# Kernel optimization log

Measured on AMD Instinct MI355X. Metric: run time of the kernel, lower is better.

Reference implementation:

```python
import jax, jax.numpy as jnp
import numpy as np

N = 100000   # num_nodes
E = 1600000  # num_edges
R = 8        # num_rels
B = 4        # num_bases
D = 64       # inp_dim = h_dim = out_dim


def setup_inputs() -> dict:
    key = jax.random.key(0)
    ks = jax.random.split(key, 16)
    s = 1.0 / np.sqrt(D)
    inp = {
        'h': jax.random.normal(ks[0], (N, D), jnp.float32),
        'src': jax.random.randint(ks[1], (E,), 0, N),
        'dst': jax.random.randint(ks[2], (E,), 0, N),
        'etype': jax.random.randint(ks[3], (E,), 0, R),
        'norm': jax.random.uniform(ks[4], (E, 1), jnp.float32),
    }
    for i in range(3):  # i2h, hidden, h2o layers (basis decomposition)
        inp[f'bases{i}'] = jax.random.normal(ks[5 + 2 * i], (B, D, D), jnp.float32) * s
        inp[f'wcomp{i}'] = jax.random.normal(ks[6 + 2 * i], (R, B), jnp.float32) * s
    inp['dec_w1'] = jax.random.normal(ks[11], (D, D), jnp.float32) * s
    inp['dec_b1'] = jnp.zeros((D,), jnp.float32)
    inp['dec_w2'] = jax.random.normal(ks[12], (D, 1), jnp.float32) * s
    inp['dec_b2'] = jnp.zeros((1,), jnp.float32)
    return inp


def rgcn_layer(h, src, dst, etype, norm, bases, wcomp, activate):
    # basis decomposition: W_r = sum_b wcomp[r,b] * bases[b]
    W = jnp.einsum('rb,bio->rio', wcomp, bases)           # [R, D, D]
    # transform all nodes under every relation (dense GEMM), then gather per edge
    Ht = jnp.einsum('ni,rio->rno', h, W).reshape(R * N, -1)  # [R*N, D]
    msg = Ht[etype * N + src] * norm                      # [E, D] gather + norm
    out = jax.ops.segment_sum(msg, dst, num_segments=N)   # scatter-add to dst
    return jax.nn.relu(out) if activate else out


def reference(h, src, dst, etype, norm, bases0, wcomp0, bases1, wcomp1,
              bases2, wcomp2, dec_w1, dec_b1, dec_w2, dec_b2):
    # EncoderRGCN: i2h (relu) -> hidden (relu) -> h2o (no activation)
    h1 = rgcn_layer(h, src, dst, etype, norm, bases0, wcomp0, True)
    h2 = rgcn_layer(h1, src, dst, etype, norm, bases1, wcomp1, True)
    henc = rgcn_layer(h2, src, dst, etype, norm, bases2, wcomp2, False)
    # AttributeDecoder: Linear -> ReLU -> Linear(reconstruct_dim=1)
    d1 = jax.nn.relu(henc @ dec_w1 + dec_b1)
    rec = (d1 @ dec_w2 + dec_b2).squeeze()                # [N]
    return rec, henc
```

## Files before the change

kernel.cpp:

```cpp
#include <hip/hip_runtime.h>

typedef _Float16 half8 __attribute__((ext_vector_type(8)));
typedef _Float16 half4 __attribute__((ext_vector_type(4)));
typedef _Float16 half2v __attribute__((ext_vector_type(2)));
typedef float floatx4 __attribute__((ext_vector_type(4)));

constexpr int NN = 100000;
constexpr int EE = 1600000;
constexpr int NBK = 196;
constexpr int CHUNK = 3125;
constexpr int CAPB = 12288;
constexpr int NDCAP = 48;

__global__ __launch_bounds__(512) void k_part(const int* __restrict__ dst,
                                              const int* __restrict__ src,
                                              const int* __restrict__ etype,
                                              const float* __restrict__ norm,
                                              int* __restrict__ gcur,
                                              int2* __restrict__ part) {
  __shared__ int2 ldata[CHUNK];
  __shared__ unsigned char lbkt[CHUNK];
  __shared__ int lhist[NBK], lbase[NBK + 1], lcur[NBK], gbase[NBK];
  __shared__ int sh[256];
  const int tid = threadIdx.x;
  const int e0 = blockIdx.x * CHUNK;

  if (tid < NBK) lhist[tid] = 0;
  __syncthreads();
  for (int i = tid; i < CHUNK; i += 512)
    atomicAdd(&lhist[dst[e0 + i] >> 9], 1);
  __syncthreads();
  {
    const int v = (tid < NBK) ? lhist[tid] : 0;
    if (tid < 256) sh[tid] = v;
    __syncthreads();
    int run = v;
    for (int d = 1; d < 256; d <<= 1) {
      const int t = (tid >= d && tid < 256) ? sh[tid - d] : 0;
      __syncthreads();
      run += t;
      if (tid < 256) sh[tid] = run;
      __syncthreads();
    }
    if (tid < NBK) {
      lbase[tid] = run - v;
      lcur[tid] = 0;
      gbase[tid] = tid * CAPB + atomicAdd(&gcur[tid], v);
    }
    if (tid == 0) lbase[NBK] = CHUNK;
  }
  __syncthreads();
  for (int i = tid; i < CHUNK; i += 512) {
    const int e = e0 + i;
    const int d = dst[e], s = src[e], et = etype[e];
    const _Float16 nh = (_Float16)norm[e];
    const unsigned short n16 = __builtin_bit_cast(unsigned short, nh);
    const int bk = d >> 9;
    const int pos = lbase[bk] + atomicAdd(&lcur[bk], 1);
    ldata[pos] = make_int2((d << 15) | (s >> 2), (s & 3) | (et << 2) | ((int)n16 << 5));
    lbkt[pos] = (unsigned char)bk;
  }
  __syncthreads();
  for (int i = tid; i < CHUNK; i += 512) {
    const int bk = (int)lbkt[i];
    part[gbase[bk] + (i - lbase[bk])] = ldata[i];
  }
}

__global__ __launch_bounds__(1024) void k_part2(const int* __restrict__ gcur,
                                                const int2* __restrict__ part,
                                                int* __restrict__ off,
                                                int2* __restrict__ em) {
  __shared__ int hcnt[512];
  __shared__ int wred[16];
  __shared__ int swsum[8];
  const int tid = threadIdx.x;
  const int bk = blockIdx.x;
  const int nb0 = bk << 9;
  const int2* __restrict__ pp = part + (size_t)bk * CAPB;

  {
    int pv = (tid < bk) ? gcur[tid] : 0;
    for (int d = 32; d > 0; d >>= 1) pv += __shfl_down(pv, d);
    if ((tid & 63) == 0) wred[tid >> 6] = pv;
  }
  if (tid < 512) hcnt[tid] = 0;
  __syncthreads();
  int base = 0;
#pragma unroll
  for (int w = 0; w < 16; ++w) base += wred[w];
  const int cntb = gcur[bk];

  for (int i = tid; i < cntb; i += 1024)
    atomicAdd(&hcnt[(((unsigned)pp[i].x) >> 15) & 511], 1);
  __syncthreads();
  const int v = (tid < 512) ? hcnt[tid] : 0;
  int incl = v;
  for (int d = 1; d < 64; d <<= 1) {
    const int t = __shfl_up(incl, d);
    if ((tid & 63) >= d) incl += t;
  }
  if (tid < 512 && (tid & 63) == 63) swsum[tid >> 6] = incl;
  __syncthreads();
  if (tid < 512) {
    int pre = 0;
    for (int w = 0; w < (tid >> 6); ++w) pre += swsum[w];
    const int excl = pre + incl - v;
    const int n = nb0 + tid;
    if (n < NN) off[n] = base + excl;
    hcnt[tid] = excl;
  }
  if (bk == NBK - 1 && tid == 0) off[NN] = EE;
  __syncthreads();
  for (int i = tid; i < cntb; i += 1024) {
    const int2 r = pp[i];
    const int d = ((unsigned)r.x) >> 15;
    const int s = ((r.x & 0x7FFF) << 2) | (r.y & 3);
    const int et = (r.y >> 2) & 7;
    const unsigned short n16 = (unsigned short)((r.y >> 5) & 0xFFFF);
    const float nf = (float)__builtin_bit_cast(_Float16, n16);
    const int pos = atomicAdd(&hcnt[d & 511], 1);
    em[base + pos] = make_int2(((d & 15) << 23) | (et << 20) | s, __float_as_int(nf));
  }
}


__global__ __launch_bounds__(256) void k_prep(const float* __restrict__ h,
                                              _Float16* __restrict__ hh,
                                              const float* __restrict__ b0,
                                              const float* __restrict__ b1,
                                              const float* __restrict__ b2,
                                              _Float16* __restrict__ bbt,
                                              int* __restrict__ gcur) {
  const int bx = blockIdx.x;
  if (bx == 0 && threadIdx.x < NBK) gcur[threadIdx.x] = 0;
  if (bx < 6250) {
    const int i = bx * 256 + threadIdx.x;
    const float4 v = *(const float4*)&h[(size_t)i * 4];
    half4 o = {(_Float16)v.x, (_Float16)v.y, (_Float16)v.z, (_Float16)v.w};
    *(half4*)&hh[(size_t)i * 4] = o;
  } else {
    const int g = (bx - 6250) >> 6;
    const int idx = ((bx - 6250) & 63) * 256 + threadIdx.x;
    const float* bases = (g == 0) ? b0 : (g == 1) ? b1 : b2;
    const int o = idx >> 8, k = idx & 255;
    const int b = k >> 6, i = k & 63;
    bbt[g * 16384 + idx] = (_Float16)bases[b * 4096 + i * 64 + o];
  }
}

__global__ __launch_bounds__(256, 8) void k_layer(const _Float16* __restrict__ hh,
                                                  const int* __restrict__ off,
                                                  const int2* __restrict__ em,
                                                  const float* __restrict__ wcomp,
                                                  const _Float16* __restrict__ bbt,
                                                  _Float16* __restrict__ out16,
                                                  float* __restrict__ out32) {
  __shared__ _Float16 Ash[16 * 264];
  __shared__ int  ems_s[16 * NDCAP];
  __shared__ int2 ems_c[16 * NDCAP];
  __shared__ float4 wcs[8];
  __shared__ int offs[17];
  __shared__ int ovf;
  const int tid = threadIdx.x;
  const int lane = tid & 63;
  const int wv = tid >> 6;
  const int n0 = blockIdx.x * 16;

  if (tid < 17) offs[tid] = off[n0 + tid];
  if (tid == 0) ovf = 0;
  if (tid < 8) wcs[tid] = ((const float4*)wcomp)[tid];
  {
    const int4 z4 = make_int4(0, 0, 0, 0);
    int4* zs = (int4*)ems_s;
    int4* zc = (int4*)ems_c;
    if (tid < 192) zs[tid] = z4;
    for (int i = tid; i < 384; i += 256) zc[i] = z4;
  }
  __syncthreads();

  const int e0 = offs[0];
  const int len = offs[16] - e0;
  for (int i = tid; i < len; i += 256) {
    const int g = e0 + i;
    const int2 r = em[g];
    const int lo = (r.x >> 23) & 15;
    const int rank = g - offs[lo];
    const int et = (r.x >> 20) & 7;
    const int s = r.x & 0xFFFFF;
    const float nf = __int_as_float(r.y);
    const float4 w = wcs[et];
    const _Float16 c0 = (_Float16)(nf * w.x), c1 = (_Float16)(nf * w.y);
    const _Float16 c2 = (_Float16)(nf * w.z), c3 = (_Float16)(nf * w.w);
    const half2v p01 = {c0, c1}, p23 = {c2, c3};
    if (rank < NDCAP) {
      ems_s[lo * NDCAP + rank] = s;
      ems_c[lo * NDCAP + rank] = make_int2(
          __builtin_bit_cast(int, p01), __builtin_bit_cast(int, p23));
    } else ovf = 1;
  }
  __syncthreads();

#define LOADB(mm, bb, hv)                                                      \
  {                                                                            \
    const int4* sp4_ = (const int4*)&ems_s[(mm) * NDCAP + (bb) * 16 + eg * 8]; \
    const int4 sa_ = sp4_[0], sb_ = sp4_[1];                                   \
    hv[0] = hp[(unsigned)sa_.x * 32u + fl];                                    \
    hv[1] = hp[(unsigned)sa_.y * 32u + fl];                                    \
    hv[2] = hp[(unsigned)sa_.z * 32u + fl];                                    \
    hv[3] = hp[(unsigned)sa_.w * 32u + fl];                                    \
    hv[4] = hp[(unsigned)sb_.x * 32u + fl];                                    \
    hv[5] = hp[(unsigned)sb_.y * 32u + fl];                                    \
    hv[6] = hp[(unsigned)sb_.z * 32u + fl];                                    \
    hv[7] = hp[(unsigned)sb_.w * 32u + fl];                                    \
  }

#define FMAQ(mm, bb, hv, aq)                                                   \
  {                                                                            \
    const int4* cp4_ = (const int4*)&ems_c[(mm) * NDCAP + (bb) * 16 + eg * 8]; \
    _Pragma("unroll")                                                          \
    for (int k_ = 0; k_ < 4; ++k_) {                                           \
      const int4 c_ = cp4_[k_];                                                \
      const half2v pa01_ = __builtin_bit_cast(half2v, c_.x);                   \
      const half2v pa23_ = __builtin_bit_cast(half2v, c_.y);                   \
      const half2v pb01_ = __builtin_bit_cast(half2v, c_.z);                   \
      const half2v pb23_ = __builtin_bit_cast(half2v, c_.w);                   \
      aq[0] = aq[0] + hv[2 * k_] * __builtin_shufflevector(pa01_, pa01_, 0, 0);\
      aq[1] = aq[1] + hv[2 * k_] * __builtin_shufflevector(pa01_, pa01_, 1, 1);\
      aq[2] = aq[2] + hv[2 * k_] * __builtin_shufflevector(pa23_, pa23_, 0, 0);\
      aq[3] = aq[3] + hv[2 * k_] * __builtin_shufflevector(pa23_, pa23_, 1, 1);\
      aq[0] = aq[0] + hv[2 * k_ + 1] * __builtin_shufflevector(pb01_, pb01_, 0, 0);\
      aq[1] = aq[1] + hv[2 * k_ + 1] * __builtin_shufflevector(pb01_, pb01_, 1, 1);\
      aq[2] = aq[2] + hv[2 * k_ + 1] * __builtin_shufflevector(pb23_, pb23_, 0, 0);\
      aq[3] = aq[3] + hv[2 * k_ + 1] * __builtin_shufflevector(pb23_, pb23_, 1, 1);\
    }                                                                          \
  }

  if (!ovf) {
    const int fl = lane & 31;
    const int eg = lane >> 5;
    const half2v* __restrict__ hp = (const half2v*)hh;
    const int mb = wv * 4;
    const int oA = offs[mb], oB = offs[mb + 1], oC = offs[mb + 2],
              oD = offs[mb + 3], oE = offs[mb + 4];
    const int c0n = oB - oA, c1n = oC - oB, c2n = oD - oC, c3n = oE - oD;
    const int nb0_ = (c0n > 0) ? ((c0n + 15) >> 4) : 1;
    const int nb1_ = (c1n > 0) ? ((c1n + 15) >> 4) : 1;
    const int nb2_ = (c2n > 0) ? ((c2n + 15) >> 4) : 1;
    const int nb3_ = (c3n > 0) ? ((c3n + 15) >> 4) : 1;

    half2v acc[4][4];
#pragma unroll
    for (int q = 0; q < 4; ++q)
#pragma unroll
      for (int i = 0; i < 4; ++i) acc[q][i] = half2v{0, 0};

    half2v hvA[8], hvB[8];
    LOADB(mb, 0, hvA);
#pragma unroll
    for (int q = 0; q < 4; ++q) {
      const int m = mb + q;
      const int nbq = (q == 0) ? nb0_ : (q == 1) ? nb1_ : (q == 2) ? nb2_ : nb3_;
      if (q < 3) {
        if (q & 1) LOADB(m + 1, 0, hvA) else LOADB(m + 1, 0, hvB)
      }
      if (q & 1) FMAQ(m, 0, hvB, acc[q]) else FMAQ(m, 0, hvA, acc[q])
      for (int b = 1; b < nbq; ++b) {
        if (q & 1) {
          LOADB(m, b, hvB) FMAQ(m, b, hvB, acc[q])
        } else {
          LOADB(m, b, hvA) FMAQ(m, b, hvA, acc[q])
        }
      }
    }
#pragma unroll
    for (int q = 0; q < 4; ++q) {
      const int m = mb + q;
#pragma unroll
      for (int i = 0; i < 4; ++i)
        acc[q][i] = acc[q][i] + __builtin_bit_cast(half2v,
            __shfl_xor(__builtin_bit_cast(int, acc[q][i]), 32));
      if (eg == 0) {
        _Float16* ar = &Ash[m * 264];
        *(half2v*)&ar[0 * 64 + 2 * fl] = acc[q][0];
        *(half2v*)&ar[1 * 64 + 2 * fl] = acc[q][1];
        *(half2v*)&ar[2 * 64 + 2 * fl] = acc[q][2];
        *(half2v*)&ar[3 * 64 + 2 * fl] = acc[q][3];
      }
    }
  } else {
    const _Float16* hl = hh + lane;
    for (int q = 0; q < 4; ++q) {
      const int m = wv * 4 + q;
      const int p0 = offs[m], p1 = offs[m + 1];
      float a0 = 0.f, a1 = 0.f, a2 = 0.f, a3 = 0.f;
      for (int p = p0; p < p1; p += 8) {
#pragma unroll
        for (int j = 0; j < 8; ++j) {
          const bool live = (p + j < p1);
          const int idx = live ? p + j : p1 - 1;
          const int2 mm = em[idx];
          const float hv = (float)hl[(size_t)(mm.x & 0xFFFFF) << 6];
          const float wn = live ? __int_as_float(mm.y) : 0.f;
          const float4 w = wcs[(mm.x >> 20) & 7];
          const float t = wn * hv;
          a0 = fmaf(t, w.x, a0); a1 = fmaf(t, w.y, a1);
          a2 = fmaf(t, w.z, a2); a3 = fmaf(t, w.w, a3);
        }
      }
      _Float16* ar = &Ash[m * 264];
      ar[lane]       = (_Float16)a0;
      ar[64 + lane]  = (_Float16)a1;
      ar[128 + lane] = (_Float16)a2;
      ar[192 + lane] = (_Float16)a3;
    }
  }
  __syncthreads();

  const int col = lane & 15;
  const int quad = lane >> 4;
  const int obase = wv * 16 + col;
  const _Float16* ap = &Ash[col * 264 + quad * 8];
  const _Float16* bp = &bbt[(size_t)obase * 256 + quad * 8];
  floatx4 acc2 = {0.f, 0.f, 0.f, 0.f};
#pragma unroll
  for (int s = 0; s < 8; ++s) {
    const half8 af = *(const half8*)(ap + s * 32);
    const half8 bf = *(const half8*)(bp + s * 32);
    acc2 = __builtin_amdgcn_mfma_f32_16x16x32_f16(af, bf, acc2, 0, 0, 0);
  }
  if (out16) {
#pragma unroll
    for (int r = 0; r < 4; ++r) {
      const float c = fmaxf(acc2[r], 0.f);
      out16[(size_t)(n0 + quad * 4 + r) * 64 + obase] = (_Float16)c;
    }
  } else {
#pragma unroll
    for (int r = 0; r < 4; ++r) {
      out32[(size_t)(n0 + quad * 4 + r) * 64 + obase] = acc2[r];
    }
  }
#undef LOADB
#undef FMAQ
}

__global__ __launch_bounds__(256) void k_dec(const float* __restrict__ henc,
                                             const float* __restrict__ w1,
                                             const float* __restrict__ b1,
                                             const float* __restrict__ w2,
                                             const float* __restrict__ b2,
                                             float* __restrict__ rec) {
  __shared__ float w1s[64 * 64];
  __shared__ float hs[16 * 68];
  const int tid = threadIdx.x;
  for (int r = tid; r < 1024; r += 256)
    *(float4*)&w1s[r * 4] = *(const float4*)&w1[r * 4];
  const int og = tid & 15;
  const int nl = tid >> 4;
  const float4 wv2 = *(const float4*)&w2[og * 4];
  const float4 bv1 = *(const float4*)&b1[og * 4];
  const float b2v = b2[0];
  for (int t0 = blockIdx.x * 16; t0 < NN; t0 += gridDim.x * 16) {
    __syncthreads();
    {
      const float4 hv = *(const float4*)&henc[(size_t)t0 * 64 + tid * 4];
      *(float4*)&hs[(tid >> 4) * 68 + (tid & 15) * 4] = hv;
    }
    __syncthreads();
    float4 acc = bv1;
    const float* hr = &hs[nl * 68];
#pragma unroll 8
    for (int i = 0; i < 64; ++i) {
      const float hv = hr[i];
      const float4 wv = *(const float4*)&w1s[i * 64 + og * 4];
      acc.x = fmaf(hv, wv.x, acc.x); acc.y = fmaf(hv, wv.y, acc.y);
      acc.z = fmaf(hv, wv.z, acc.z); acc.w = fmaf(hv, wv.w, acc.w);
    }
    acc.x = fmaxf(acc.x, 0.f); acc.y = fmaxf(acc.y, 0.f);
    acc.z = fmaxf(acc.z, 0.f); acc.w = fmaxf(acc.w, 0.f);
    float v = acc.x * wv2.x + acc.y * wv2.y + acc.z * wv2.z + acc.w * wv2.w;
    v += __shfl_xor(v, 1); v += __shfl_xor(v, 2);
    v += __shfl_xor(v, 4); v += __shfl_xor(v, 8);
    if (og == 0) rec[t0 + nl] = v + b2v;
  }
}


extern "C" void kernel_launch(void* const* d_in, const int* in_sizes, int n_in,
                              void* d_out, int out_size, void* d_ws, size_t ws_size,
                              hipStream_t stream) {
  const float* h     = (const float*)d_in[0];
  const int*   src   = (const int*)d_in[1];
  const int*   dst   = (const int*)d_in[2];
  const int*   etype = (const int*)d_in[3];
  const float* norm  = (const float*)d_in[4];
  const float* bases[3] = {(const float*)d_in[5], (const float*)d_in[7], (const float*)d_in[9]};
  const float* wcomp[3] = {(const float*)d_in[6], (const float*)d_in[8], (const float*)d_in[10]};
  const float* dw1 = (const float*)d_in[11];
  const float* db1 = (const float*)d_in[12];
  const float* dw2 = (const float*)d_in[13];
  const float* db2 = (const float*)d_in[14];

  float* rec  = (float*)d_out;
  float* henc = (float*)d_out + NN;

  char* ws = (char*)d_ws;
  int*      off    = (int*)(ws + 0);
  int*      gcur   = (int*)(ws + 400512);
  int2*     em     = (int2*)(ws + 402560);
  _Float16* hh     = (_Float16*)(ws + 13202560);
  _Float16* h1f    = (_Float16*)(ws + 26002560);
  _Float16* h2f    = (_Float16*)(ws + 38802560);
  _Float16* bbt    = (_Float16*)(ws + 51602560);
  int2*     part   = (int2*)h1f;

  k_prep<<<6250 + 192, 256, 0, stream>>>(h, hh, bases[0], bases[1], bases[2], bbt, gcur);

  k_part<<<512, 512, 0, stream>>>(dst, src, etype, norm, gcur, part);
  k_part2<<<NBK, 1024, 0, stream>>>(gcur, part, off, em);

  k_layer<<<NN / 16, 256, 0, stream>>>(hh,  off, em, wcomp[0], bbt,         h1f, nullptr);
  k_layer<<<NN / 16, 256, 0, stream>>>(h1f, off, em, wcomp[1], bbt + 16384, h2f, nullptr);
  k_layer<<<NN / 16, 256, 0, stream>>>(h2f, off, em, wcomp[2], bbt + 32768, nullptr, henc);

  k_dec<<<1024, 256, 0, stream>>>(henc, dw1, db1, dw2, db2, rec);
}
```

Before: 322.5 us.

## Triple-buffer edge gathers across nodes with fully unrolled static schedule

Replaces the per-node loop, which kept two gather buffers in flight, with a fully unrolled schedule that keeps three register buffers in flight. Node batches interleave, so the gather loads for one batch overlap the FMAs of another. The new code handles at most three 16-edge batches per node, which relies on the NDCAP=48 limit and the overflow fallback. Launch bounds drop from 8 to 6 waves per unit to make room for the extra registers, trading occupancy for more memory-level parallelism in each wave.

```diff
diff --git a/kernel.cpp b/kernel.cpp
--- a/kernel.cpp
+++ b/kernel.cpp
@@ -149,7 +149,7 @@
   }
 }
 
-__global__ __launch_bounds__(256, 8) void k_layer(const _Float16* __restrict__ hh,
+__global__ __launch_bounds__(256, 6) void k_layer(const _Float16* __restrict__ hh,
                                                   const int* __restrict__ off,
                                                   const int2* __restrict__ em,
                                                   const float* __restrict__ wcomp,
@@ -201,39 +201,43 @@
   }
   __syncthreads();
 
-#define LOADB(mm, bb, hv)                                                      \
+#define LOADB(mm, bb, P)                                                       \
   {                                                                            \
     const int4* sp4_ = (const int4*)&ems_s[(mm) * NDCAP + (bb) * 16 + eg * 8]; \
     const int4 sa_ = sp4_[0], sb_ = sp4_[1];                                   \
-    hv[0] = hp[(unsigned)sa_.x * 32u + fl];                                    \
-    hv[1] = hp[(unsigned)sa_.y * 32u + fl];                                    \
-    hv[2] = hp[(unsigned)sa_.z * 32u + fl];                                    \
-    hv[3] = hp[(unsigned)sa_.w * 32u + fl];                                    \
-    hv[4] = hp[(unsigned)sb_.x * 32u + fl];                                    \
-    hv[5] = hp[(unsigned)sb_.y * 32u + fl];                                    \
-    hv[6] = hp[(unsigned)sb_.z * 32u + fl];                                    \
-    hv[7] = hp[(unsigned)sb_.w * 32u + fl];                                    \
-  }
-
-#define FMAQ(mm, bb, hv, aq)                                                   \
+    P##0 = hp[(unsigned)sa_.x * 32u + fl];                                     \
+    P##1 = hp[(unsigned)sa_.y * 32u + fl];                                     \
+    P##2 = hp[(unsigned)sa_.z * 32u + fl];                                     \
+    P##3 = hp[(unsigned)sa_.w * 32u + fl];                                     \
+    P##4 = hp[(unsigned)sb_.x * 32u + fl];                                     \
+    P##5 = hp[(unsigned)sb_.y * 32u + fl];                                     \
+    P##6 = hp[(unsigned)sb_.z * 32u + fl];                                     \
+    P##7 = hp[(unsigned)sb_.w * 32u + fl];                                     \
+  }
+
+#define FMA2(hx, hy, cc, qi)                                                   \
+  {                                                                            \
+    const half2v pa01_ = __builtin_bit_cast(half2v, cc.x);                     \
+    const half2v pa23_ = __builtin_bit_cast(half2v, cc.y);                     \
+    const half2v pb01_ = __builtin_bit_cast(half2v, cc.z);                     \
+    const half2v pb23_ = __builtin_bit_cast(half2v, cc.w);                     \
+    acc[qi][0] = acc[qi][0] + hx * __builtin_shufflevector(pa01_, pa01_, 0, 0);\
+    acc[qi][1] = acc[qi][1] + hx * __builtin_shufflevector(pa01_, pa01_, 1, 1);\
+    acc[qi][2] = acc[qi][2] + hx * __builtin_shufflevector(pa23_, pa23_, 0, 0);\
+    acc[qi][3] = acc[qi][3] + hx * __builtin_shufflevector(pa23_, pa23_, 1, 1);\
+    acc[qi][0] = acc[qi][0] + hy * __builtin_shufflevector(pb01_, pb01_, 0, 0);\
+    acc[qi][1] = acc[qi][1] + hy * __builtin_shufflevector(pb01_, pb01_, 1, 1);\
+    acc[qi][2] = acc[qi][2] + hy * __builtin_shufflevector(pb23_, pb23_, 0, 0);\
+    acc[qi][3] = acc[qi][3] + hy * __builtin_shufflevector(pb23_, pb23_, 1, 1);\
+  }
+
+#define FMAQ(mm, bb, P, qi)                                                    \
   {                                                                            \
     const int4* cp4_ = (const int4*)&ems_c[(mm) * NDCAP + (bb) * 16 + eg * 8]; \
-    _Pragma("unroll")                                                          \
-    for (int k_ = 0; k_ < 4; ++k_) {                                           \
-      const int4 c_ = cp4_[k_];                                                \
-      const half2v pa01_ = __builtin_bit_cast(half2v, c_.x);                   \
-      const half2v pa23_ = __builtin_bit_cast(half2v, c_.y);                   \
-      const half2v pb01_ = __builtin_bit_cast(half2v, c_.z);                   \
-      const half2v pb23_ = __builtin_bit_cast(half2v, c_.w);                   \
-      aq[0] = aq[0] + hv[2 * k_] * __builtin_shufflevector(pa01_, pa01_, 0, 0);\
-      aq[1] = aq[1] + hv[2 * k_] * __builtin_shufflevector(pa01_, pa01_, 1, 1);\
-      aq[2] = aq[2] + hv[2 * k_] * __builtin_shufflevector(pa23_, pa23_, 0, 0);\
-      aq[3] = aq[3] + hv[2 * k_] * __builtin_shufflevector(pa23_, pa23_, 1, 1);\
-      aq[0] = aq[0] + hv[2 * k_ + 1] * __builtin_shufflevector(pb01_, pb01_, 0, 0);\
-      aq[1] = aq[1] + hv[2 * k_ + 1] * __builtin_shufflevector(pb01_, pb01_, 1, 1);\
-      aq[2] = aq[2] + hv[2 * k_ + 1] * __builtin_shufflevector(pb23_, pb23_, 0, 0);\
-      aq[3] = aq[3] + hv[2 * k_ + 1] * __builtin_shufflevector(pb23_, pb23_, 1, 1);\
-    }                                                                          \
+    const int4 c0_ = cp4_[0]; FMA2(P##0, P##1, c0_, qi)                        \
+    const int4 c1_ = cp4_[1]; FMA2(P##2, P##3, c1_, qi)                        \
+    const int4 c2_ = cp4_[2]; FMA2(P##4, P##5, c2_, qi)                        \
+    const int4 c3_ = cp4_[3]; FMA2(P##6, P##7, c3_, qi)                        \
   }
 
   if (!ovf) {
@@ -244,10 +248,8 @@
     const int oA = offs[mb], oB = offs[mb + 1], oC = offs[mb + 2],
               oD = offs[mb + 3], oE = offs[mb + 4];
     const int c0n = oB - oA, c1n = oC - oB, c2n = oD - oC, c3n = oE - oD;
-    const int nb0_ = (c0n > 0) ? ((c0n + 15) >> 4) : 1;
-    const int nb1_ = (c1n > 0) ? ((c1n + 15) >> 4) : 1;
-    const int nb2_ = (c2n > 0) ? ((c2n + 15) >> 4) : 1;
-    const int nb3_ = (c3n > 0) ? ((c3n + 15) >> 4) : 1;
+    const bool v1_0 = c0n > 16, v1_1 = c1n > 16, v1_2 = c2n > 16, v1_3 = c3n > 16;
+    const bool v2_0 = c0n > 32, v2_1 = c1n > 32, v2_2 = c2n > 32, v2_3 = c3n > 32;
 
     half2v acc[4][4];
 #pragma unroll
@@ -255,24 +257,35 @@
 #pragma unroll
       for (int i = 0; i < 4; ++i) acc[q][i] = half2v{0, 0};
 
-    half2v hvA[8], hvB[8];
-    LOADB(mb, 0, hvA);
-#pragma unroll
-    for (int q = 0; q < 4; ++q) {
-      const int m = mb + q;
-      const int nbq = (q == 0) ? nb0_ : (q == 1) ? nb1_ : (q == 2) ? nb2_ : nb3_;
-      if (q < 3) {
-        if (q & 1) LOADB(m + 1, 0, hvA) else LOADB(m + 1, 0, hvB)
-      }
-      if (q & 1) FMAQ(m, 0, hvB, acc[q]) else FMAQ(m, 0, hvA, acc[q])
-      for (int b = 1; b < nbq; ++b) {
-        if (q & 1) {
-          LOADB(m, b, hvB) FMAQ(m, b, hvB, acc[q])
-        } else {
-          LOADB(m, b, hvA) FMAQ(m, b, hvA, acc[q])
-        }
-      }
-    }
+    half2v x0, x1, x2, x3, x4, x5, x6, x7;
+    half2v y0, y1, y2, y3, y4, y5, y6, y7;
+    half2v z0, z1, z2, z3, z4, z5, z6, z7;
+
+    LOADB(mb + 0, 0, x)
+    LOADB(mb + 1, 0, y)
+    LOADB(mb + 2, 0, z)
+    FMAQ(mb + 0, 0, x, 0)
+    LOADB(mb + 3, 0, x)
+    FMAQ(mb + 1, 0, y, 1)
+    if (v1_0) LOADB(mb + 0, 1, y)
+    FMAQ(mb + 2, 0, z, 2)
+    if (v1_1) LOADB(mb + 1, 1, z)
+    FMAQ(mb + 3, 0, x, 3)
+    if (v1_2) LOADB(mb + 2, 1, x)
+    if (v1_0) FMAQ(mb + 0, 1, y, 0)
+    if (v1_3) LOADB(mb + 3, 1, y)
+    if (v1_1) FMAQ(mb + 1, 1, z, 1)
+    if (v2_0) LOADB(mb + 0, 2, z)
+    if (v1_2) FMAQ(mb + 2, 1, x, 2)
+    if (v2_1) LOADB(mb + 1, 2, x)
+    if (v1_3) FMAQ(mb + 3, 1, y, 3)
+    if (v2_2) LOADB(mb + 2, 2, y)
+    if (v2_0) FMAQ(mb + 0, 2, z, 0)
+    if (v2_3) LOADB(mb + 3, 2, z)
+    if (v2_1) FMAQ(mb + 1, 2, x, 1)
+    if (v2_2) FMAQ(mb + 2, 2, y, 2)
+    if (v2_3) FMAQ(mb + 3, 2, z, 3)
+
 #pragma unroll
     for (int q = 0; q < 4; ++q) {
       const int m = mb + q;
@@ -342,6 +355,7 @@
     }
   }
 #undef LOADB
+#undef FMA2
 #undef FMAQ
 }
 
```

Result: slower. 841.6 us (+161.0%).

## Replace two-pass bucketed CSR build with atomic histogram, scan, and placement

Applied to the files above, without the earlier changes.

Drops the two-stage bucket partition (per-block local sort into 196 dst buckets, then a per-bucket counting sort) that built the dst-sorted edge list. In its place are a global atomic degree histogram, a two-kernel prefix scan, and an atomic-cursor placement kernel. The new path trades shared-memory staging and coalesced writes for simpler kernels. It adds many global atomics on the degree and cursor arrays and scattered 8-byte writes to em. Edge order within a node is no longer deterministic, so floating-point accumulation order can vary between runs.

```diff
diff --git a/kernel.cpp b/kernel.cpp
--- a/kernel.cpp
+++ b/kernel.cpp
@@ -7,120 +7,68 @@
 
 constexpr int NN = 100000;
 constexpr int EE = 1600000;
-constexpr int NBK = 196;
-constexpr int CHUNK = 3125;
-constexpr int CAPB = 12288;
 constexpr int NDCAP = 48;
 
-__global__ __launch_bounds__(512) void k_part(const int* __restrict__ dst,
-                                              const int* __restrict__ src,
-                                              const int* __restrict__ etype,
-                                              const float* __restrict__ norm,
-                                              int* __restrict__ gcur,
-                                              int2* __restrict__ part) {
-  __shared__ int2 ldata[CHUNK];
-  __shared__ unsigned char lbkt[CHUNK];
-  __shared__ int lhist[NBK], lbase[NBK + 1], lcur[NBK], gbase[NBK];
-  __shared__ int sh[256];
+
+__global__ __launch_bounds__(256) void k_hist(const int* __restrict__ dst,
+                                              int* __restrict__ deg) {
+  for (int e = blockIdx.x * 256 + threadIdx.x; e < EE; e += gridDim.x * 256)
+    atomicAdd(&deg[dst[e]], 1);
+}
+
+__global__ __launch_bounds__(1024) void k_scanA(const int* __restrict__ deg,
+                                                int* __restrict__ st,
+                                                int* __restrict__ bsum) {
+  __shared__ int wsum[16];
   const int tid = threadIdx.x;
-  const int e0 = blockIdx.x * CHUNK;
-
-  if (tid < NBK) lhist[tid] = 0;
-  __syncthreads();
-  for (int i = tid; i < CHUNK; i += 512)
-    atomicAdd(&lhist[dst[e0 + i] >> 9], 1);
-  __syncthreads();
-  {
-    const int v = (tid < NBK) ? lhist[tid] : 0;
-    if (tid < 256) sh[tid] = v;
-    __syncthreads();
-    int run = v;
-    for (int d = 1; d < 256; d <<= 1) {
-      const int t = (tid >= d && tid < 256) ? sh[tid - d] : 0;
-      __syncthreads();
-      run += t;
-      if (tid < 256) sh[tid] = run;
-      __syncthreads();
-    }
-    if (tid < NBK) {
-      lbase[tid] = run - v;
-      lcur[tid] = 0;
-      gbase[tid] = tid * CAPB + atomicAdd(&gcur[tid], v);
-    }
-    if (tid == 0) lbase[NBK] = CHUNK;
-  }
-  __syncthreads();
-  for (int i = tid; i < CHUNK; i += 512) {
-    const int e = e0 + i;
-    const int d = dst[e], s = src[e], et = etype[e];
-    const _Float16 nh = (_Float16)norm[e];
-    const unsigned short n16 = __builtin_bit_cast(unsigned short, nh);
-    const int bk = d >> 9;
-    const int pos = lbase[bk] + atomicAdd(&lcur[bk], 1);
-    ldata[pos] = make_int2((d << 15) | (s >> 2), (s & 3) | (et << 2) | ((int)n16 << 5));
-    lbkt[pos] = (unsigned char)bk;
-  }
-  __syncthreads();
-  for (int i = tid; i < CHUNK; i += 512) {
-    const int bk = (int)lbkt[i];
-    part[gbase[bk] + (i - lbase[bk])] = ldata[i];
-  }
-}
-
-__global__ __launch_bounds__(1024) void k_part2(const int* __restrict__ gcur,
-                                                const int2* __restrict__ part,
-                                                int* __restrict__ off,
-                                                int2* __restrict__ em) {
-  __shared__ int hcnt[512];
-  __shared__ int wred[16];
-  __shared__ int swsum[8];
-  const int tid = threadIdx.x;
-  const int bk = blockIdx.x;
-  const int nb0 = bk << 9;
-  const int2* __restrict__ pp = part + (size_t)bk * CAPB;
-
-  {
-    int pv = (tid < bk) ? gcur[tid] : 0;
-    for (int d = 32; d > 0; d >>= 1) pv += __shfl_down(pv, d);
-    if ((tid & 63) == 0) wred[tid >> 6] = pv;
-  }
-  if (tid < 512) hcnt[tid] = 0;
-  __syncthreads();
-  int base = 0;
-#pragma unroll
-  for (int w = 0; w < 16; ++w) base += wred[w];
-  const int cntb = gcur[bk];
-
-  for (int i = tid; i < cntb; i += 1024)
-    atomicAdd(&hcnt[(((unsigned)pp[i].x) >> 15) & 511], 1);
-  __syncthreads();
-  const int v = (tid < 512) ? hcnt[tid] : 0;
+  const int i = blockIdx.x * 1024 + tid;
+  const int v = (i < NN) ? deg[i] : 0;
   int incl = v;
   for (int d = 1; d < 64; d <<= 1) {
     const int t = __shfl_up(incl, d);
     if ((tid & 63) >= d) incl += t;
   }
-  if (tid < 512 && (tid & 63) == 63) swsum[tid >> 6] = incl;
-  __syncthreads();
-  if (tid < 512) {
-    int pre = 0;
-    for (int w = 0; w < (tid >> 6); ++w) pre += swsum[w];
-    const int excl = pre + incl - v;
-    const int n = nb0 + tid;
-    if (n < NN) off[n] = base + excl;
-    hcnt[tid] = excl;
-  }
-  if (bk == NBK - 1 && tid == 0) off[NN] = EE;
-  __syncthreads();
-  for (int i = tid; i < cntb; i += 1024) {
-    const int2 r = pp[i];
-    const int d = ((unsigned)r.x) >> 15;
-    const int s = ((r.x & 0x7FFF) << 2) | (r.y & 3);
-    const int et = (r.y >> 2) & 7;
-    const unsigned short n16 = (unsigned short)((r.y >> 5) & 0xFFFF);
-    const float nf = (float)__builtin_bit_cast(_Float16, n16);
-    const int pos = atomicAdd(&hcnt[d & 511], 1);
-    em[base + pos] = make_int2(((d & 15) << 23) | (et << 20) | s, __float_as_int(nf));
+  if ((tid & 63) == 63) wsum[tid >> 6] = incl;
+  __syncthreads();
+  int pre = 0;
+  for (int w = 0; w < (tid >> 6); ++w) pre += wsum[w];
+  if (i < NN) st[i] = pre + incl - v;
+  if (tid == 1023) bsum[blockIdx.x] = pre + incl;
+}
+
+__global__ __launch_bounds__(1024) void k_scanB(const int* __restrict__ bsum,
+                                                int* __restrict__ st,
+                                                int* __restrict__ cur) {
+  __shared__ int wr[16];
+  const int tid = threadIdx.x;
+  const int b = blockIdx.x;
+  int pv = (tid < b) ? bsum[tid] : 0;
+  for (int d = 32; d > 0; d >>= 1) pv += __shfl_down(pv, d);
+  if ((tid & 63) == 0) wr[tid >> 6] = pv;
+  __syncthreads();
+  int base = 0;
+#pragma unroll
+  for (int w = 0; w < 16; ++w) base += wr[w];
+  const int i = b * 1024 + tid;
+  if (i < NN) {
+    const int s = st[i] + base;
+    st[i] = s;
+    cur[i] = s;
+  }
+  if (b == 0 && tid == 0) st[NN] = EE;
+}
+
+__global__ __launch_bounds__(256) void k_place(const int* __restrict__ dst,
+                                               const int* __restrict__ src,
+                                               const int* __restrict__ etype,
+                                               const float* __restrict__ norm,
+                                               int* __restrict__ cur,
+                                               int2* __restrict__ em) {
+  for (int e = blockIdx.x * 256 + threadIdx.x; e < EE; e += gridDim.x * 256) {
+    const int d = dst[e];
+    const int pos = atomicAdd(&cur[d], 1);
+    em[pos] = make_int2(((d & 15) << 23) | (etype[e] << 20) | src[e],
+                        __float_as_int(norm[e]));
   }
 }
 
@@ -131,21 +79,23 @@
                                               const float* __restrict__ b1,
                                               const float* __restrict__ b2,
                                               _Float16* __restrict__ bbt,
-                                              int* __restrict__ gcur) {
+                                              int* __restrict__ deg) {
   const int bx = blockIdx.x;
-  if (bx == 0 && threadIdx.x < NBK) gcur[threadIdx.x] = 0;
   if (bx < 6250) {
     const int i = bx * 256 + threadIdx.x;
     const float4 v = *(const float4*)&h[(size_t)i * 4];
     half4 o = {(_Float16)v.x, (_Float16)v.y, (_Float16)v.z, (_Float16)v.w};
     *(half4*)&hh[(size_t)i * 4] = o;
-  } else {
+  } else if (bx < 6442) {
     const int g = (bx - 6250) >> 6;
     const int idx = ((bx - 6250) & 63) * 256 + threadIdx.x;
     const float* bases = (g == 0) ? b0 : (g == 1) ? b1 : b2;
     const int o = idx >> 8, k = idx & 255;
     const int b = k >> 6, i = k & 63;
     bbt[g * 16384 + idx] = (_Float16)bases[b * 4096 + i * 64 + o];
+  } else {
+    const int idx = (bx - 6442) * 256 + threadIdx.x;
+    ((int4*)deg)[idx] = make_int4(0, 0, 0, 0);
   }
 }
 
@@ -406,23 +356,26 @@
   float* henc = (float*)d_out + NN;
 
   char* ws = (char*)d_ws;
-  int*      off    = (int*)(ws + 0);
-  int*      gcur   = (int*)(ws + 400512);
+  int*      st     = (int*)(ws + 0);
   int2*     em     = (int2*)(ws + 402560);
   _Float16* hh     = (_Float16*)(ws + 13202560);
   _Float16* h1f    = (_Float16*)(ws + 26002560);
   _Float16* h2f    = (_Float16*)(ws + 38802560);
   _Float16* bbt    = (_Float16*)(ws + 51602560);
-  int2*     part   = (int2*)h1f;
-
-  k_prep<<<6250 + 192, 256, 0, stream>>>(h, hh, bases[0], bases[1], bases[2], bbt, gcur);
-
-  k_part<<<512, 512, 0, stream>>>(dst, src, etype, norm, gcur, part);
-  k_part2<<<NBK, 1024, 0, stream>>>(gcur, part, off, em);
-
-  k_layer<<<NN / 16, 256, 0, stream>>>(hh,  off, em, wcomp[0], bbt,         h1f, nullptr);
-  k_layer<<<NN / 16, 256, 0, stream>>>(h1f, off, em, wcomp[1], bbt + 16384, h2f, nullptr);
-  k_layer<<<NN / 16, 256, 0, stream>>>(h2f, off, em, wcomp[2], bbt + 32768, nullptr, henc);
+  int*      deg    = (int*)(ws + 26002560);
+  int*      cur    = (int*)(ws + 26403968);
+  int*      bsum   = (int*)(ws + 26803968);
+
+  k_prep<<<6250 + 192 + 98, 256, 0, stream>>>(h, hh, bases[0], bases[1], bases[2], bbt, deg);
+
+  k_hist<<<2048, 256, 0, stream>>>(dst, deg);
+  k_scanA<<<98, 1024, 0, stream>>>(deg, st, bsum);
+  k_scanB<<<98, 1024, 0, stream>>>(bsum, st, cur);
+  k_place<<<2048, 256, 0, stream>>>(dst, src, etype, norm, cur, em);
+
+  k_layer<<<NN / 16, 256, 0, stream>>>(hh,  st, em, wcomp[0], bbt,         h1f, nullptr);
+  k_layer<<<NN / 16, 256, 0, stream>>>(h1f, st, em, wcomp[1], bbt + 16384, h2f, nullptr);
+  k_layer<<<NN / 16, 256, 0, stream>>>(h2f, st, em, wcomp[2], bbt + 32768, nullptr, henc);
 
   k_dec<<<1024, 256, 0, stream>>>(henc, dw1, db1, dw2, db2, rec);
 }
```

Result: slower. 462.0 us (+43.3%).
